# Kernel tuning notes

Hardware: AMD Instinct MI355X
Metric: run time of the kernel (lower is better)

The kernel has to match this reference:

```python
import jax, jax.numpy as jnp
import numpy as np

IN_FEATURES = 4096
OUT_FEATURES = 11008
GROUPSIZE = 128


def setup_inputs() -> dict:
    key = jax.random.key(0)
    k_x, k_w, k_s, k_z = jax.random.split(key, 4)
    x = jax.random.normal(k_x, (4, 2048, IN_FEATURES), dtype=jnp.float32)
    # each int32 word packs 8 int4 nibbles along the in_features axis
    packed_weight = jax.random.randint(
        k_w, (IN_FEATURES // 8, OUT_FEATURES), 0, 2147483647, dtype=jnp.int32
    )
    n_groups = IN_FEATURES // GROUPSIZE
    scales = jax.random.uniform(k_s, (OUT_FEATURES, n_groups), dtype=jnp.float32)
    zeros = jax.random.uniform(k_z, (OUT_FEATURES, n_groups), dtype=jnp.float32)
    return {
        "x": x,
        "packed_weight": packed_weight,
        "scales": scales,
        "zeros": zeros,
        "groupsize": GROUPSIZE,
    }


def reference(x, packed_weight, scales, zeros, groupsize):
    # Unpack int4 nibbles: element i of in_features lives in packed_weight[i//8],
    # nibble (i % 8) (little-endian nibble order).
    in_features = packed_weight.shape[0] * 8
    shifts = (jnp.arange(8, dtype=jnp.int32) * 4)  # [8]
    q = (packed_weight[:, None, :] >> shifts[None, :, None]) & 0xF  # [in//8, 8, out]
    q = q.reshape(in_features, -1).astype(jnp.float32)  # [in, out]
    # Per-group dequant: w = (q - zero) * scale, groups along in_features.
    s = jnp.repeat(scales.T, groupsize, axis=0)  # [in, out]
    z = jnp.repeat(zeros.T, groupsize, axis=0)   # [in, out]
    w = (q - z) * s
    return jnp.einsum("bsi,io->bso", x, w)
```

## Files before the change

### kernel.cpp

```cpp
#include <hip/hip_runtime.h>


#define M_DIM 8192
#define K_DIM 4096
#define N_DIM 11008
#define BM 256
#define BN 128
#define BK 64
#define NKT (K_DIM / BK)

typedef unsigned short u16;
typedef __bf16 bf16x8 __attribute__((ext_vector_type(8)));
typedef float floatx4 __attribute__((ext_vector_type(4)));
typedef u16 u16x8 __attribute__((ext_vector_type(8)));
typedef u16 u16x4 __attribute__((ext_vector_type(4)));

typedef __attribute__((address_space(1))) const void* gcvp;
typedef __attribute__((address_space(3))) void* svp;

static __device__ __forceinline__ u16 f2b(float f) {
  union { float f; unsigned u; } v;
  v.f = f;
  unsigned r = v.u + 0x7FFFu + ((v.u >> 16) & 1u);
  return (u16)(r >> 16);
}

__global__ __launch_bounds__(256) void cvt_x_kernel(const float* __restrict__ x,
                                                    u16* __restrict__ xb) {
  int i = blockIdx.x * 256 + threadIdx.x;
  const int n4 = (M_DIM * K_DIM) / 4;
  const int stride = 2048 * 256;
  for (; i < n4; i += stride) {
    const float4 v = reinterpret_cast<const float4*>(x)[i];
    u16x4 r;
    r[0] = f2b(v.x); r[1] = f2b(v.y); r[2] = f2b(v.z); r[3] = f2b(v.w);
    reinterpret_cast<u16x4*>(xb)[i] = r;
  }
}

__global__ __launch_bounds__(256) void dequant_w_kernel(const int* __restrict__ pw,
                                                        const float* __restrict__ sc,
                                                        const float* __restrict__ zr,
                                                        u16* __restrict__ wbt) {
  __shared__ int tile[64][65];
  const int t = threadIdx.x;
  const int o0 = blockIdx.x * 64;
  const int kw0 = blockIdx.y * 64;
#pragma unroll
  for (int r = 0; r < 16; ++r) {
    const int kw = r * 4 + (t >> 6);
    const int o = t & 63;
    tile[kw][o] = pw[(kw0 + kw) * N_DIM + o0 + o];
  }
  __syncthreads();
  const int kwl = t & 63;
  const int g = (kw0 + kwl) >> 4;
  const int obase = (t >> 6) * 16;
  for (int it = 0; it < 16; ++it) {
    const int ol = obase + it;
    const int o = o0 + ol;
    const float s = sc[o * 32 + g];
    const float z = zr[o * 32 + g];
    const float b = -z * s;
    const int word = tile[kwl][ol];
    u16x8 r;
#pragma unroll
    for (int j = 0; j < 8; ++j) {
      const float q = (float)((word >> (4 * j)) & 0xF);
      r[j] = f2b(fmaf(q, s, b));
    }
    *reinterpret_cast<u16x8*>(&wbt[(size_t)o * K_DIM + (size_t)(kw0 + kwl) * 8]) = r;
  }
}


#define WAITV(n)                                             \
  asm volatile("s_waitcnt vmcnt(" #n ")" ::: "memory");      \
  __builtin_amdgcn_sched_barrier(0)
#define BAR __builtin_amdgcn_s_barrier()

__global__ __launch_bounds__(256, 2) void gemm_kernel(const u16* __restrict__ xb,
                                                      const u16* __restrict__ wbt,
                                                      float* __restrict__ out) {
  __shared__ __align__(16) u16 lds[(BM + BN) * BK];

  const int tid = threadIdx.x;
  const int w = tid >> 6;
  const int l = tid & 63;
  const int wm = w >> 1;
  const int wn = w & 1;

  const int bid = blockIdx.x;
  const int wg = (bid & 7) * 344 + (bid >> 3);
  const int NT = N_DIM / BN;
  const int m0 = (wg / NT) * BM;
  const int n0 = (wg % NT) * BN;

  const int sr = tid >> 3;
  const int scc = ((tid & 7) ^ (sr & 7)) * 8;
  const u16* srcA = xb + (size_t)(m0 + sr) * K_DIM + scc;
  const u16* srcB = wbt + (size_t)(n0 + sr) * K_DIM + scc;

#define STAGEU(op, u, t)                                                       \
  __builtin_amdgcn_global_load_lds(                                            \
      gcvp(((op) ? srcB : srcA) + (size_t)((u) * 32) * K_DIM + (t) * 64),      \
      svp(&lds[(op) * 16384 + ((u) * 32 + w * 8) * 64]), 16, 0, 0)

  const int swz = ((l >> 4) ^ (l & 7)) * 8;
  const int baseA = (wm * 128 + (l & 15)) * 64 + swz;
  const int baseB = 16384 + (wn * 64 + (l & 15)) * 64 + swz;
  const u16* lp = &lds[0];

  bf16x8 a[4][2], b0[2][2], b1[2][2];

#define LDA(S)                                                                          \
  do {                                                                                  \
    _Pragma("unroll") for (int _m = 0; _m < 4; ++_m) {                                  \
      const int _e = baseA + ((S) * 4 + _m) * 1024;                                     \
      a[_m][0] = *reinterpret_cast<const bf16x8*>(&lp[_e]);                             \
      a[_m][1] = *reinterpret_cast<const bf16x8*>(&lp[_e ^ 32]);                        \
    }                                                                                   \
  } while (0)
#define LDB(BA, U)                                                                      \
  do {                                                                                  \
    _Pragma("unroll") for (int _n = 0; _n < 2; ++_n) {                                  \
      const int _e = baseB + ((U) * 2 + _n) * 1024;                                     \
      BA[_n][0] = *reinterpret_cast<const bf16x8*>(&lp[_e]);                            \
      BA[_n][1] = *reinterpret_cast<const bf16x8*>(&lp[_e ^ 32]);                       \
    }                                                                                   \
  } while (0)

  floatx4 acc[8][4] = {};

#define QMFMA(S, BA, U)                                                                 \
  do {                                                                                  \
    __builtin_amdgcn_s_setprio(1);                                                     \
    _Pragma("unroll") for (int _m = 0; _m < 4; ++_m)                                    \
      _Pragma("unroll") for (int _n = 0; _n < 2; ++_n)                                  \
        _Pragma("unroll") for (int _k = 0; _k < 2; ++_k)                                \
          acc[(S) * 4 + _m][(U) * 2 + _n] = __builtin_amdgcn_mfma_f32_16x16x32_bf16(    \
              a[_m][_k], BA[_n][_k], acc[(S) * 4 + _m][(U) * 2 + _n], 0, 0, 0);         \
    __builtin_amdgcn_s_setprio(0);                                                     \
  } while (0)

  STAGEU(0, 0, 0); STAGEU(0, 1, 0); STAGEU(0, 4, 0); STAGEU(0, 5, 0);
  STAGEU(1, 0, 0); STAGEU(1, 2, 0);
  STAGEU(1, 1, 0); STAGEU(1, 3, 0);
  STAGEU(0, 2, 0); STAGEU(0, 3, 0); STAGEU(0, 6, 0); STAGEU(0, 7, 0);

  for (int t = 0; t < NKT - 1; ++t) {
    WAITV(6); BAR;
    LDA(0);
    LDB(b0, 0);
    QMFMA(0, b0, 0);
    WAITV(4); BAR;
    STAGEU(0, 0, t + 1); STAGEU(0, 1, t + 1); STAGEU(0, 4, t + 1); STAGEU(0, 5, t + 1);
    STAGEU(1, 0, t + 1); STAGEU(1, 2, t + 1);
    LDB(b1, 1);
    QMFMA(0, b1, 1);
    WAITV(6); BAR;
    STAGEU(1, 1, t + 1); STAGEU(1, 3, t + 1);
    LDA(1);
    QMFMA(1, b0, 0);
    BAR;
    STAGEU(0, 2, t + 1); STAGEU(0, 3, t + 1); STAGEU(0, 6, t + 1); STAGEU(0, 7, t + 1);
    QMFMA(1, b1, 1);
  }

  {
    WAITV(6); BAR;
    LDA(0);
    LDB(b0, 0);
    QMFMA(0, b0, 0);
    WAITV(4); BAR;
    LDB(b1, 1);
    QMFMA(0, b1, 1);
    WAITV(0); BAR;
    LDA(1);
    QMFMA(1, b0, 0);
    QMFMA(1, b1, 1);
  }

  const int orow0 = m0 + wm * 128 + (l >> 4) * 4;
  const int ocol0 = n0 + wn * 64 + (l & 15);
#pragma unroll
  for (int mi = 0; mi < 8; ++mi)
#pragma unroll
    for (int j = 0; j < 4; ++j) {
      float* op = out + (size_t)(orow0 + mi * 16 + j) * N_DIM + ocol0;
#pragma unroll
      for (int ni = 0; ni < 4; ++ni) op[ni * 16] = acc[mi][ni][j];
    }
}

__global__ __launch_bounds__(256) void gemm_naive(const float* __restrict__ x,
                                                  const int* __restrict__ pw,
                                                  const float* __restrict__ sc,
                                                  const float* __restrict__ zr,
                                                  float* __restrict__ out) {
  const int idx = blockIdx.x * 256 + threadIdx.x;
  if (idx >= M_DIM * N_DIM) return;
  const int m = idx / N_DIM, o = idx % N_DIM;
  const float* xr = x + (size_t)m * K_DIM;
  float acc = 0.f;
  for (int g = 0; g < 32; ++g) {
    const float s = sc[o * 32 + g];
    const float z = zr[o * 32 + g];
    const float b = -z * s;
    for (int kw = g * 16; kw < g * 16 + 16; ++kw) {
      const int word = pw[kw * N_DIM + o];
#pragma unroll
      for (int j = 0; j < 8; ++j) {
        const float q = (float)((word >> (4 * j)) & 0xF);
        acc += xr[kw * 8 + j] * fmaf(q, s, b);
      }
    }
  }
  out[idx] = acc;
}

extern "C" void kernel_launch(void* const* d_in, const int* in_sizes, int n_in,
                              void* d_out, int out_size, void* d_ws, size_t ws_size,
                              hipStream_t stream) {
  (void)in_sizes; (void)n_in; (void)out_size;
  const float* x = (const float*)d_in[0];
  const int* pw = (const int*)d_in[1];
  const float* sc = (const float*)d_in[2];
  const float* zr = (const float*)d_in[3];
  float* out = (float*)d_out;

  const size_t need = ((size_t)M_DIM * K_DIM + (size_t)N_DIM * K_DIM) * 2;
  if (ws_size >= need) {
    u16* xb = (u16*)d_ws;
    u16* wbt = xb + (size_t)M_DIM * K_DIM;
    cvt_x_kernel<<<2048, 256, 0, stream>>>(x, xb);
    dequant_w_kernel<<<dim3(N_DIM / 64, (K_DIM / 8) / 64), 256, 0, stream>>>(pw, sc, zr, wbt);
    gemm_kernel<<<(M_DIM / BM) * (N_DIM / BN), 256, 0, stream>>>(xb, wbt, out);
  } else {
    gemm_naive<<<(M_DIM * N_DIM + 255) / 256, 256, 0, stream>>>(x, pw, sc, zr, out);
  }
}
```

Before: 697.2 us.

## Shrink GEMM tile to 128x128 with simpler single-buffer pipeline and higher occupancy

Halves the M tile from 256 to 128, so each wave computes a 64x64 sub-tile with a 4x4 accumulator array, and raises launch bounds to 3 blocks per CU. The interleaved partial-stage pipeline with fine-grained vmcnt waits is replaced by a simpler loop: wait for all loads, read the whole LDS tile into registers, run half the MFMAs, barrier, issue the next tile's global-to-LDS loads, then run the other half. The aim is to hide latency through more resident blocks rather than intra-block overlap. The tradeoff is lower arithmetic intensity per tile, more global traffic for the weight operand, and a full vmcnt(0) stall at every iteration.

After: 924.1 us. 1.33x slower.

```diff
diff --git a/kernel.cpp b/kernel.cpp
--- a/kernel.cpp
+++ b/kernel.cpp
@@ -4,7 +4,7 @@
 #define M_DIM 8192
 #define K_DIM 4096
 #define N_DIM 11008
-#define BM 256
+#define BM 128
 #define BN 128
 #define BK 64
 #define NKT (K_DIM / BK)
@@ -74,12 +74,12 @@
 }
 
 
-#define WAITV(n)                                             \
-  asm volatile("s_waitcnt vmcnt(" #n ")" ::: "memory");      \
+#define WAITV0                                               \
+  asm volatile("s_waitcnt vmcnt(0)" ::: "memory");           \
   __builtin_amdgcn_sched_barrier(0)
 #define BAR __builtin_amdgcn_s_barrier()
 
-__global__ __launch_bounds__(256, 2) void gemm_kernel(const u16* __restrict__ xb,
+__global__ __launch_bounds__(256, 3) void gemm_kernel(const u16* __restrict__ xb,
                                                       const u16* __restrict__ wbt,
                                                       float* __restrict__ out) {
   __shared__ __align__(16) u16 lds[(BM + BN) * BK];
@@ -91,7 +91,7 @@
   const int wn = w & 1;
 
   const int bid = blockIdx.x;
-  const int wg = (bid & 7) * 344 + (bid >> 3);
+  const int wg = (bid & 7) * 688 + (bid >> 3);
   const int NT = N_DIM / BN;
   const int m0 = (wg / NT) * BM;
   const int n0 = (wg % NT) * BN;
@@ -104,87 +104,70 @@
 #define STAGEU(op, u, t)                                                       \
   __builtin_amdgcn_global_load_lds(                                            \
       gcvp(((op) ? srcB : srcA) + (size_t)((u) * 32) * K_DIM + (t) * 64),      \
-      svp(&lds[(op) * 16384 + ((u) * 32 + w * 8) * 64]), 16, 0, 0)
+      svp(&lds[(op) * 8192 + ((u) * 32 + w * 8) * 64]), 16, 0, 0)
+
+#define STAGEALL(t)                                                            \
+  do {                                                                         \
+    STAGEU(0, 0, t); STAGEU(0, 1, t); STAGEU(0, 2, t); STAGEU(0, 3, t);        \
+    STAGEU(1, 0, t); STAGEU(1, 1, t); STAGEU(1, 2, t); STAGEU(1, 3, t);        \
+  } while (0)
 
   const int swz = ((l >> 4) ^ (l & 7)) * 8;
-  const int baseA = (wm * 128 + (l & 15)) * 64 + swz;
-  const int baseB = 16384 + (wn * 64 + (l & 15)) * 64 + swz;
+  const int baseA = (wm * 64 + (l & 15)) * 64 + swz;
+  const int baseB = 8192 + (wn * 64 + (l & 15)) * 64 + swz;
   const u16* lp = &lds[0];
 
-  bf16x8 a[4][2], b0[2][2], b1[2][2];
-
-#define LDA(S)                                                                          \
+  bf16x8 a[4][2], b[4][2];
+
+#define LDALL                                                                           \
   do {                                                                                  \
     _Pragma("unroll") for (int _m = 0; _m < 4; ++_m) {                                  \
-      const int _e = baseA + ((S) * 4 + _m) * 1024;                                     \
+      const int _e = baseA + _m * 1024;                                                 \
       a[_m][0] = *reinterpret_cast<const bf16x8*>(&lp[_e]);                             \
       a[_m][1] = *reinterpret_cast<const bf16x8*>(&lp[_e ^ 32]);                        \
     }                                                                                   \
-  } while (0)
-#define LDB(BA, U)                                                                      \
-  do {                                                                                  \
-    _Pragma("unroll") for (int _n = 0; _n < 2; ++_n) {                                  \
-      const int _e = baseB + ((U) * 2 + _n) * 1024;                                     \
-      BA[_n][0] = *reinterpret_cast<const bf16x8*>(&lp[_e]);                            \
-      BA[_n][1] = *reinterpret_cast<const bf16x8*>(&lp[_e ^ 32]);                       \
+    _Pragma("unroll") for (int _n = 0; _n < 4; ++_n) {                                  \
+      const int _e = baseB + _n * 1024;                                                 \
+      b[_n][0] = *reinterpret_cast<const bf16x8*>(&lp[_e]);                             \
+      b[_n][1] = *reinterpret_cast<const bf16x8*>(&lp[_e ^ 32]);                        \
     }                                                                                   \
   } while (0)
 
-  floatx4 acc[8][4] = {};
-
-#define QMFMA(S, BA, U)                                                                 \
+  floatx4 acc[4][4] = {};
+
+#define QMFMA(U)                                                                        \
   do {                                                                                  \
     __builtin_amdgcn_s_setprio(1);                                                     \
     _Pragma("unroll") for (int _m = 0; _m < 4; ++_m)                                    \
       _Pragma("unroll") for (int _n = 0; _n < 2; ++_n)                                  \
         _Pragma("unroll") for (int _k = 0; _k < 2; ++_k)                                \
-          acc[(S) * 4 + _m][(U) * 2 + _n] = __builtin_amdgcn_mfma_f32_16x16x32_bf16(    \
-              a[_m][_k], BA[_n][_k], acc[(S) * 4 + _m][(U) * 2 + _n], 0, 0, 0);         \
+          acc[_m][(U) * 2 + _n] = __builtin_amdgcn_mfma_f32_16x16x32_bf16(              \
+              a[_m][_k], b[(U) * 2 + _n][_k], acc[_m][(U) * 2 + _n], 0, 0, 0);          \
     __builtin_amdgcn_s_setprio(0);                                                     \
   } while (0)
 
-  STAGEU(0, 0, 0); STAGEU(0, 1, 0); STAGEU(0, 4, 0); STAGEU(0, 5, 0);
-  STAGEU(1, 0, 0); STAGEU(1, 2, 0);
-  STAGEU(1, 1, 0); STAGEU(1, 3, 0);
-  STAGEU(0, 2, 0); STAGEU(0, 3, 0); STAGEU(0, 6, 0); STAGEU(0, 7, 0);
-
+  STAGEALL(0);
+
+#pragma unroll 2
   for (int t = 0; t < NKT - 1; ++t) {
-    WAITV(6); BAR;
-    LDA(0);
-    LDB(b0, 0);
-    QMFMA(0, b0, 0);
-    WAITV(4); BAR;
-    STAGEU(0, 0, t + 1); STAGEU(0, 1, t + 1); STAGEU(0, 4, t + 1); STAGEU(0, 5, t + 1);
-    STAGEU(1, 0, t + 1); STAGEU(1, 2, t + 1);
-    LDB(b1, 1);
-    QMFMA(0, b1, 1);
-    WAITV(6); BAR;
-    STAGEU(1, 1, t + 1); STAGEU(1, 3, t + 1);
-    LDA(1);
-    QMFMA(1, b0, 0);
+    WAITV0; BAR;
+    LDALL;
+    QMFMA(0);
     BAR;
-    STAGEU(0, 2, t + 1); STAGEU(0, 3, t + 1); STAGEU(0, 6, t + 1); STAGEU(0, 7, t + 1);
-    QMFMA(1, b1, 1);
-  }
-
+    STAGEALL(t + 1);
+    QMFMA(1);
+  }
   {
-    WAITV(6); BAR;
-    LDA(0);
-    LDB(b0, 0);
-    QMFMA(0, b0, 0);
-    WAITV(4); BAR;
-    LDB(b1, 1);
-    QMFMA(0, b1, 1);
-    WAITV(0); BAR;
-    LDA(1);
-    QMFMA(1, b0, 0);
-    QMFMA(1, b1, 1);
-  }
-
-  const int orow0 = m0 + wm * 128 + (l >> 4) * 4;
+    WAITV0; BAR;
+    LDALL;
+    QMFMA(0);
+    QMFMA(1);
+  }
+
+  const int orow0 = m0 + wm * 64 + (l >> 4) * 4;
   const int ocol0 = n0 + wn * 64 + (l & 15);
 #pragma unroll
-  for (int mi = 0; mi < 8; ++mi)
+  for (int mi = 0; mi < 4; ++mi)
 #pragma unroll
     for (int j = 0; j < 4; ++j) {
       float* op = out + (size_t)(orow0 + mi * 16 + j) * N_DIM + ocol0;
```
